# Kernel tuning notes

Measured on AMD Instinct MI355X. Metric: run time of the kernel, lower is better.

Reference implementation:

```python
import jax, jax.numpy as jnp
import numpy as np

B = 32          # claims
EVI = 5         # evidences per claim
L = 130         # max_len
H = 768         # bert_hidden_dim
K = 21          # n gaussian kernels
NL = 3          # num_labels
N = B * EVI


def _kernel_mus(n):
    mu = [1.0]
    bs = 2.0 / (n - 1)
    mu.append(1.0 - bs / 2.0)
    for i in range(1, n - 1):
        mu.append(mu[i] - bs)
    return mu


def _kernel_sigmas(n):
    return [0.001] + [0.1] * (n - 1)

MU = jnp.asarray(_kernel_mus(K), jnp.float32)      # [K]
SIGMA = jnp.asarray(_kernel_sigmas(K), jnp.float32)  # [K]


def _l2norm(x):
    # F.normalize(p=2, dim=-1, eps=1e-12)
    return x / jnp.maximum(jnp.linalg.norm(x, axis=-1, keepdims=True), 1e-12)


def _kernel_pool(sim, attn_d):
    # sim: [P, Q, D] cosine sims; attn_d: [P, D] doc mask -> [P, Q, K]
    pv = jnp.exp(-0.5 * ((sim[..., None] - MU) / SIGMA) ** 2) * attn_d[:, None, :, None]
    return pv.sum(axis=2)


def setup_inputs() -> dict:
    key = jax.random.key(0)
    ks = jax.random.split(key, 10)
    def p(k, shape, s=0.02):
        return jax.random.normal(k, shape, jnp.float32) * s
    return dict(
        hiddens=jax.random.normal(ks[0], (N, L, H), jnp.float32),
        pooled=jax.random.normal(ks[1], (N, H), jnp.float32),
        msk=jnp.ones((N, L), jnp.int32),
        seg=jax.random.randint(ks[2], (N, L), 0, 2, dtype=jnp.int32),
        W_att=p(ks[3], (1, K)), b_att=jnp.zeros((1,), jnp.float32),
        W_sel=p(ks[4], (1, K)), b_sel=jnp.zeros((1,), jnp.float32),
        Wg1=p(ks[5], (128, 2 * H)), bg1=jnp.zeros((128,), jnp.float32),
        Wg2=p(ks[6], (1, 128)), bg2=jnp.zeros((1,), jnp.float32),
        Wd=p(ks[7], (NL, 2 * H)), bd=jnp.zeros((NL,), jnp.float32),
    )


def reference(hiddens, pooled, msk, seg, W_att, b_att, W_sel, b_sel,
              Wg1, bg1, Wg2, bg2, Wd, bd):
    mask_text = msk.astype(jnp.float32).at[:, 0].set(0.0)       # [N,L] zero CLS
    segf = seg.astype(jnp.float32)
    mask_claim = (1.0 - segf) * mask_text
    mask_ev = segf * mask_text

    hn = _l2norm(hiddens)                                        # [N,L,H]

    # --- evidence selection: claim-vs-evidence kernel pooling within each row ---
    sim = jnp.einsum('nqh,ndh->nqd', hn, hn)                     # [N,L,L]
    ps = _kernel_pool(sim, mask_ev)                              # [N,L,K]
    lps = jnp.log(jnp.clip(ps, 1e-10, None)) * mask_claim[:, :, None]
    lps = lps.sum(axis=1) / (mask_claim.sum(axis=1, keepdims=True) + 1e-10)  # [N,K]
    sel = lps @ W_sel.T + b_sel                                  # [N,1]
    select_prob = jax.nn.softmax(sel.reshape(B, EVI, 1), axis=1)

    hb = hiddens.reshape(B, EVI, L, H)
    hnb = hn.reshape(B, EVI, L, H)
    mb = mask_text.reshape(B, EVI, L)
    pb = pooled.reshape(B, EVI, H)

    def proj_gat(x):
        return jnp.maximum(x @ Wg1.T + bg1, 0.0) @ Wg2.T + bg2

    # --- GAT-style aggregation; only the denoised branch feeds the output ---
    de_list = []
    for i in range(EVI):
        own_n = hnb[:, i]                                        # [B,L,H]
        own_m = jnp.repeat(mb[:, i], EVI, axis=0)                # [B*EVI,L]
        sim_i = jnp.einsum('beqh,bdh->beqd', hnb, own_n).reshape(B * EVI, L, L)
        ps_i = _kernel_pool(sim_i, own_m)                        # [B*EVI,L,K]
        score = (jnp.log(jnp.clip(ps_i, 1e-10, None)) @ W_att.T + b_att)[..., 0]
        score = jnp.where(mb.reshape(B * EVI, L) > 0, score, -10000.0)
        att = jax.nn.softmax(score, axis=1).reshape(B, EVI, L, 1)
        denoise = (att * hb).sum(axis=2)                         # [B,EVI,H]
        own_inp = jnp.broadcast_to(pb[:, i:i + 1], (B, EVI, H))
        w_de = jax.nn.softmax(proj_gat(jnp.concatenate([own_inp, denoise], -1)), axis=1)
        de_list.append((denoise * w_de).sum(axis=1))             # [B,H]

    de = jnp.stack(de_list, axis=1)                              # [B,EVI,H]
    feat = jnp.concatenate([pb, de], axis=-1) @ Wd.T + bd        # [B,EVI,NL]
    class_prob = jax.nn.softmax(feat, axis=2)
    prob = (select_prob * class_prob).sum(axis=1)                # [B,NL]
    return jnp.log(prob)
```

## Files before the change

### kernel.cpp

```cpp
#include <hip/hip_runtime.h>
#include <cstdint>
#include <cstddef>

#define BB 32
#define EV 5
#define LL 130
#define HH 768
#define KK 21
#define LP 160
#define SD 136
#define SR 130

typedef __attribute__((ext_vector_type(8))) __bf16 bf16x8;
typedef __attribute__((ext_vector_type(4))) float f32x4;

__device__ __forceinline__ unsigned short f2bf(float f) {
    unsigned int u = __float_as_uint(f);
    u += 0x7FFFu + ((u >> 16) & 1u);
    return (unsigned short)(u >> 16);
}
__device__ __forceinline__ float bf2f(unsigned int s) {
    return __uint_as_float(s << 16);
}
__device__ __forceinline__ void gld_lds16(const unsigned short* g, unsigned short* l) {
    __builtin_amdgcn_global_load_lds(
        (const __attribute__((address_space(1))) unsigned int*)g,
        (__attribute__((address_space(3))) unsigned int*)l, 16, 0, 0);
}

__global__ __launch_bounds__(256) void k_prologue(const float* __restrict__ hid,
        unsigned short* __restrict__ hnbf, const float* __restrict__ wg1,
        unsigned short* __restrict__ wg1b, const float* __restrict__ pooled,
        unsigned short* __restrict__ xg) {
    int bid = blockIdx.x, tid = threadIdx.x;
    if (bid < 5200) {
        int wave = tid >> 6, lane = tid & 63;
        int r = bid * 4 + wave;
        if (r >= 160 * LL) return;
        const float4* s4 = (const float4*)(hid + (size_t)r * HH);
        float4 v0 = s4[lane], v1 = s4[lane + 64], v2 = s4[lane + 128];
        float ss = v0.x*v0.x + v0.y*v0.y + v0.z*v0.z + v0.w*v0.w
                 + v1.x*v1.x + v1.y*v1.y + v1.z*v1.z + v1.w*v1.w
                 + v2.x*v2.x + v2.y*v2.y + v2.z*v2.z + v2.w*v2.w;
        #pragma unroll
        for (int m = 1; m < 64; m <<= 1) ss += __shfl_xor(ss, m, 64);
        float sc = 1.0f / fmaxf(sqrtf(ss), 1e-12f);
        ushort4 o0, o1, o2;
        o0.x = f2bf(v0.x*sc); o0.y = f2bf(v0.y*sc); o0.z = f2bf(v0.z*sc); o0.w = f2bf(v0.w*sc);
        o1.x = f2bf(v1.x*sc); o1.y = f2bf(v1.y*sc); o1.z = f2bf(v1.z*sc); o1.w = f2bf(v1.w*sc);
        o2.x = f2bf(v2.x*sc); o2.y = f2bf(v2.y*sc); o2.z = f2bf(v2.z*sc); o2.w = f2bf(v2.w*sc);
        ushort4* d4 = (ushort4*)(hnbf + (size_t)r * HH);
        d4[lane] = o0; d4[lane + 64] = o1; d4[lane + 128] = o2;
    } else if (bid < 5968) {
        int idx = (bid - 5200) * 256 + tid;
        wg1b[idx] = f2bf(wg1[idx]);
    } else {
        int row = bid - 5968;
        int bi = row / 5;
        const float* src = pooled + (size_t)bi * HH;
        unsigned short* dst = xg + (size_t)row * 1536;
        #pragma unroll
        for (int j = 0; j < 3; j++) { int h = tid + j * 256; dst[h] = f2bf(src[h]); }
    }
}

__global__ __launch_bounds__(256) void k_sim_gemm(const unsigned short* __restrict__ hnbf,
                                                  unsigned short* __restrict__ Sg) {
    int w = blockIdx.x;
    int xcd = w & 7, slot = w >> 3;
    int b = xcd * 4 + (slot / 25);
    int ei = slot % 25;
    int e = ei / 5, i = ei % 5;
    int pair = b * 25 + ei;
    const unsigned short* A = hnbf + (size_t)(b * 5 + e) * LL * HH;
    const unsigned short* B = hnbf + (size_t)(b * 5 + i) * LL * HH;
    __shared__ unsigned short As[160 * 64];
    __shared__ unsigned short Bs[160 * 64];
    int tid = threadIdx.x, lane = tid & 63, wave = tid >> 6;
    int quad = lane >> 4, l16 = lane & 15;
    int wm = (wave & 1) * 5, wn = (wave >> 1) * 5;
    f32x4 acc[5][5];
    #pragma unroll
    for (int mt = 0; mt < 5; mt++)
        #pragma unroll
        for (int nt = 0; nt < 5; nt++) acc[mt][nt] = (f32x4){0.f, 0.f, 0.f, 0.f};

    for (int k0 = 0; k0 < HH; k0 += 64) {
        #pragma unroll
        for (int it = 0; it < 5; it++) {
            int s = tid + it * 256;
            int r = s >> 3;
            int rs = (r < LL) ? r : 0;
            int sgl = (s & 7) ^ (r & 7);
            const unsigned short* ga = A + (size_t)rs * HH + k0 + sgl * 8;
            const unsigned short* gb = B + (size_t)rs * HH + k0 + sgl * 8;
            gld_lds16(ga, &As[s * 8]);
            gld_lds16(gb, &Bs[s * 8]);
        }
        __syncthreads();
        #pragma unroll
        for (int kb = 0; kb < 2; kb++) {
            bf16x8 af[5], bfr[5];
            #pragma unroll
            for (int t = 0; t < 5; t++) {
                int ra = (wm + t) * 16 + l16;
                int rb = (wn + t) * 16 + l16;
                af[t]  = *(const bf16x8*)&As[ra * 64 + (((kb << 2) + quad) ^ (ra & 7)) * 8];
                bfr[t] = *(const bf16x8*)&Bs[rb * 64 + (((kb << 2) + quad) ^ (rb & 7)) * 8];
            }
            #pragma unroll
            for (int mt = 0; mt < 5; mt++)
                #pragma unroll
                for (int nt = 0; nt < 5; nt++)
                    acc[mt][nt] = __builtin_amdgcn_mfma_f32_16x16x32_bf16(af[mt], bfr[nt], acc[mt][nt], 0, 0, 0);
        }
        __syncthreads();
    }
    size_t base = (size_t)pair * SR * SD;
    #pragma unroll
    for (int mt = 0; mt < 5; mt++)
        #pragma unroll
        for (int nt = 0; nt < 5; nt++) {
            int R0 = (wm + mt) * 16 + quad * 4;
            int C = (wn + nt) * 16 + l16;
            if (C < SD) {
                #pragma unroll
                for (int reg = 0; reg < 4; reg++) {
                    int R = R0 + reg;
                    if (R < SR) Sg[base + (size_t)R * SD + C] = f2bf(acc[mt][nt][reg]);
                }
            }
        }
}

template <bool DIAG>
__device__ __forceinline__ void pool_body(
    int pair, int row, int lane8, bool live, int ne, int c,
    const unsigned short* __restrict__ Sg,
    const float* __restrict__ batt,
    float* __restrict__ score, float* __restrict__ selp, float* __restrict__ denp,
    const float* wdA, const float* wdE, const float* wqC,
    const float* WaL, const float* WsL, const float* CkL,
    float* redsel, float* redden) {

    const float LOG2E = 1.4426950408889634f;
    const float CA = -50.0f * LOG2E;
    const float CB = 95.0f * LOG2E;
    const float CR = -10.0f * LOG2E;
    const float C0 = -500000.0f * LOG2E;
    int tid = threadIdx.x;

    float a0[KK], a2[KK];
    #pragma unroll
    for (int k = 0; k < KK; k++) { a0[k] = 0.0f; a2[k] = 0.0f; }

    auto proc = [&](float s, int d) {
        float w = wdA[d];
        float w2 = DIAG ? wdE[d] : 0.0f;
        float pe = exp2f(fmaf(CB, s, CA * s * s));
        float rr = exp2f(CR * s);
        float sm1 = s - 1.0f;
        float e0 = exp2f(C0 * (sm1 * sm1));
        a0[0] = fmaf(w, e0, a0[0]);
        if (DIAG) a2[0] = fmaf(w2, e0, a2[0]);
        float p = pe;
        #pragma unroll
        for (int k = 1; k < KK; k++) {
            a0[k] = fmaf(w, p, a0[k]);
            if (DIAG) a2[k] = fmaf(w2, p, a2[k]);
            p *= rr;
        }
    };

    if (live) {
        const unsigned short* Srow = Sg + (size_t)pair * SR * SD + (size_t)row * SD;
        #pragma unroll
        for (int j = 0; j < 2; j++) {
            uint4 v = *(const uint4*)(Srow + lane8 * 8 + j * 64);
            int d0 = lane8 * 8 + j * 64;
            proc(bf2f(v.x & 0xFFFFu), d0 + 0); proc(bf2f(v.x >> 16), d0 + 1);
            proc(bf2f(v.y & 0xFFFFu), d0 + 2); proc(bf2f(v.y >> 16), d0 + 3);
            proc(bf2f(v.z & 0xFFFFu), d0 + 4); proc(bf2f(v.z >> 16), d0 + 5);
            proc(bf2f(v.w & 0xFFFFu), d0 + 6); proc(bf2f(v.w >> 16), d0 + 7);
        }
        proc(bf2f((unsigned int)Srow[128 + lane8]), 128 + lane8);
    }
    #pragma unroll
    for (int k = 0; k < KK; k++) {
        a0[k] += __shfl_xor(a0[k], 1, 64);
        a0[k] += __shfl_xor(a0[k], 2, 64);
        a0[k] += __shfl_xor(a0[k], 4, 64);
        if (DIAG) {
            a2[k] += __shfl_xor(a2[k], 1, 64);
            a2[k] += __shfl_xor(a2[k], 2, 64);
            a2[k] += __shfl_xor(a2[k], 4, 64);
        }
    }
    float selv = 0.0f, denv = 0.0f;
    if (live && lane8 == 0) {
        float sc = batt[0];
        #pragma unroll
        for (int k = 0; k < KK; k++)
            sc += WaL[k] * __logf(fmaxf(CkL[k] * a0[k], 1e-10f));
        score[(size_t)pair * LP + row] = sc;
        if (DIAG) {
            float cq = 0.0f;
            #pragma unroll
            for (int k = 0; k < KK; k++)
                cq += WsL[k] * __logf(fmaxf(CkL[k] * a2[k], 1e-10f));
            selv = wqC[row] * cq;
            denv = wqC[row];
        }
    }
    if (DIAG) {
        #pragma unroll
        for (int m = 8; m < 64; m <<= 1) {
            selv += __shfl_xor(selv, m, 64);
            denv += __shfl_xor(denv, m, 64);
        }
        int wave = tid >> 6, lane = tid & 63;
        if (lane == 0) { redsel[wave] = selv; redden[wave] = denv; }
        __syncthreads();
        if (tid == 0) {
            selp[ne * 5 + c] = redsel[0] + redsel[1] + redsel[2] + redsel[3];
            denp[ne * 5 + c] = redden[0] + redden[1] + redden[2] + redden[3];
        }
    }
}

__global__ __launch_bounds__(256) void k_pool(const unsigned short* __restrict__ Sg,
        const int* __restrict__ msk, const int* __restrict__ seg,
        const float* __restrict__ Watt, const float* __restrict__ batt,
        const float* __restrict__ Wsel,
        float* __restrict__ score, float* __restrict__ selp, float* __restrict__ denp) {
    __shared__ float wdA[SD], wdE[SD], wqC[SD];
    __shared__ float WaL[KK], WsL[KK], CkL[KK];
    __shared__ float redsel[4], redden[4];
    int w = blockIdx.x;
    int xcd = w & 7, slot = w >> 3;
    int b = xcd * 4 + (slot / 125);
    int rem = slot % 125;
    int ei = rem / 5, c = rem % 5;
    int e = ei / 5, i = ei % 5;
    int pair = b * 25 + ei;
    int ne = b * 5 + e, ni = b * 5 + i;
    int tid = threadIdx.x;

    if (tid < SD) {
        int d = tid;
        wdA[d] = (d >= 1 && d < LL) ? (float)msk[ni * LL + d] : 0.0f;
        float mtE = (d >= 1 && d < LL) ? (float)msk[ne * LL + d] : 0.0f;
        float sgE = (d < LL) ? (float)seg[ne * LL + d] : 0.0f;
        wdE[d] = sgE * mtE;
        wqC[d] = (1.0f - sgE) * mtE;
    }
    if (tid < KK) {
        const float LOG2E = 1.4426950408889634f;
        WaL[tid] = Watt[tid];
        WsL[tid] = Wsel[tid];
        float mu = 0.95f - 0.1f * (tid - 1);
        CkL[tid] = (tid == 0) ? 1.0f : exp2f(-50.0f * LOG2E * mu * mu);
    }
    __syncthreads();

    int row = c * 26 + (tid >> 3);
    int lane8 = tid & 7;
    bool live = (tid < 208);

    if (e == i)
        pool_body<true>(pair, row, lane8, live, ne, c, Sg, batt, score, selp, denp,
                        wdA, wdE, wqC, WaL, WsL, CkL, redsel, redden);
    else
        pool_body<false>(pair, row, lane8, live, ne, c, Sg, batt, score, selp, denp,
                         wdA, wdE, wqC, WaL, WsL, CkL, redsel, redden);
}

__global__ __launch_bounds__(64) void k_att(const float* __restrict__ score,
        const int* __restrict__ msk, float* __restrict__ attg) {
    int bid = blockIdx.x;
    int be = bid / 5, ii = bid % 5;
    int b = be / 5, e = be % 5;
    const float* srow = score + ((size_t)(b * 5 + ii) * 5 + e) * LP;
    int lane = threadIdx.x;

    float v0, v1, v2 = -1e30f;
    {
        int q = lane;
        float mt = (q >= 1 && msk[be * LL + q] != 0) ? 1.0f : 0.0f;
        v0 = (mt > 0.0f) ? srow[q] : -1e4f;
    }
    {
        int q = lane + 64;
        float mt = (msk[be * LL + q] != 0) ? 1.0f : 0.0f;
        v1 = (mt > 0.0f) ? srow[q] : -1e4f;
    }
    if (lane < 2) {
        int q = lane + 128;
        float mt = (msk[be * LL + q] != 0) ? 1.0f : 0.0f;
        v2 = (mt > 0.0f) ? srow[q] : -1e4f;
    }
    float mx = fmaxf(v0, fmaxf(v1, v2));
    #pragma unroll
    for (int m = 1; m < 64; m <<= 1) mx = fmaxf(mx, __shfl_xor(mx, m, 64));
    float e0 = __expf(v0 - mx), e1 = __expf(v1 - mx);
    float e2 = (lane < 2) ? __expf(v2 - mx) : 0.0f;
    float Z = e0 + e1 + e2;
    #pragma unroll
    for (int m = 1; m < 64; m <<= 1) Z += __shfl_xor(Z, m, 64);
    float iz = 1.0f / Z;
    attg[(size_t)bid * LL + lane] = e0 * iz;
    attg[(size_t)bid * LL + lane + 64] = e1 * iz;
    if (lane < 2) attg[(size_t)bid * LL + lane + 128] = e2 * iz;
}

__global__ __launch_bounds__(256) void k_den(const float* __restrict__ attg,
        const float* __restrict__ hid, float* __restrict__ dn,
        unsigned short* __restrict__ xg) {
    int bid = blockIdx.x;
    int be = bid / 3, j = bid % 3;
    int b = be / 5, e = be % 5;
    int tid = threadIdx.x;
    int h = j * 256 + tid;
    __shared__ float attl[5 * LL];
    for (int s = tid; s < 5 * LL; s += 256)
        attl[s] = attg[(size_t)(be * 5) * LL + s];
    __syncthreads();

    float accA[5] = {0.f, 0.f, 0.f, 0.f, 0.f};
    float accB[5] = {0.f, 0.f, 0.f, 0.f, 0.f};
    const float* hb = hid + (size_t)be * LL * HH + h;
    int q = 0;
    #pragma unroll 2
    for (; q + 4 <= LL; q += 4) {
        float h0 = hb[(size_t)(q + 0) * HH];
        float h1 = hb[(size_t)(q + 1) * HH];
        float h2 = hb[(size_t)(q + 2) * HH];
        float h3 = hb[(size_t)(q + 3) * HH];
        #pragma unroll
        for (int i = 0; i < 5; i++) {
            accA[i] = fmaf(attl[i * LL + q], h0, accA[i]);
            accB[i] = fmaf(attl[i * LL + q + 1], h1, accB[i]);
            accA[i] = fmaf(attl[i * LL + q + 2], h2, accA[i]);
            accB[i] = fmaf(attl[i * LL + q + 3], h3, accB[i]);
        }
    }
    for (; q < LL; q++) {
        float hv = hb[(size_t)q * HH];
        #pragma unroll
        for (int i = 0; i < 5; i++) accA[i] = fmaf(attl[i * LL + q], hv, accA[i]);
    }
    #pragma unroll
    for (int i = 0; i < 5; i++) {
        float v = accA[i] + accB[i];
        dn[((size_t)be * 5 + i) * HH + h] = v;
        xg[((size_t)(b * 5 + i) * 5 + e) * 1536 + HH + h] = f2bf(v);
    }
}

__global__ __launch_bounds__(256) void k_gate_gemm(const unsigned short* __restrict__ xg,
        const unsigned short* __restrict__ wg1b, float* __restrict__ cg) {
    int bid = blockIdx.x;
    int rb = bid / 3, ks = bid % 3;
    int m0 = rb * 16;
    __shared__ unsigned short As[16 * 32];
    __shared__ unsigned short Bs[128 * 32];
    int tid = threadIdx.x, lane = tid & 63, wave = tid >> 6;
    int quad = lane >> 4, l16 = lane & 15;
    f32x4 acc[2];
    acc[0] = (f32x4){0.f, 0.f, 0.f, 0.f};
    acc[1] = (f32x4){0.f, 0.f, 0.f, 0.f};

    for (int t = 0; t < 16; t++) {
        int k0 = ks * 512 + t * 32;
        if (tid < 64) {
            int row = tid >> 2, sg = tid & 3;
            *(uint4*)&As[tid * 8] = *(const uint4*)(xg + (size_t)(m0 + row) * 1536 + k0 + sg * 8);
        }
        #pragma unroll
        for (int it = 0; it < 2; it++) {
            int s = tid + it * 256;
            int row = s >> 2, sg = s & 3;
            *(uint4*)&Bs[s * 8] = *(const uint4*)(wg1b + (size_t)row * 1536 + k0 + sg * 8);
        }
        __syncthreads();
        bf16x8 af = *(const bf16x8*)&As[l16 * 32 + quad * 8];
        #pragma unroll
        for (int nt = 0; nt < 2; nt++) {
            int ct = wave * 2 + nt;
            bf16x8 bfr = *(const bf16x8*)&Bs[(ct * 16 + l16) * 32 + quad * 8];
            acc[nt] = __builtin_amdgcn_mfma_f32_16x16x32_bf16(af, bfr, acc[nt], 0, 0, 0);
        }
        __syncthreads();
    }
    #pragma unroll
    for (int nt = 0; nt < 2; nt++) {
        int C = (wave * 2 + nt) * 16 + l16;
        #pragma unroll
        for (int reg = 0; reg < 4; reg++) {
            int R = m0 + quad * 4 + reg;
            atomicAdd(&cg[(size_t)R * 128 + C], acc[nt][reg]);
        }
    }
}

__global__ __launch_bounds__(256) void k_gate_epi(const float* __restrict__ cg,
        const float* __restrict__ bg1, const float* __restrict__ wg2,
        const float* __restrict__ bg2, const float* __restrict__ dn,
        const float* __restrict__ pooled, const float* __restrict__ wd,
        const float* __restrict__ bd, float* __restrict__ feat) {
    int bi = blockIdx.x;
    int b = bi / 5, ii = bi % 5;
    __shared__ float red4[4];
    __shared__ float gL[5];
    __shared__ float deL[HH];
    int tid = threadIdx.x, lane = tid & 63, wave = tid >> 6;

    for (int e = 0; e < 5; e++) {
        float v = 0.0f;
        if (tid < 128) {
            float ccv = cg[(size_t)(bi * 5 + e) * 128 + tid] + bg1[tid];
            v = wg2[tid] * fmaxf(ccv, 0.0f);
        }
        #pragma unroll
        for (int m = 1; m < 64; m <<= 1) v += __shfl_xor(v, m, 64);
        if (lane == 0) red4[wave] = v;
        __syncthreads();
        if (tid == 0) gL[e] = red4[0] + red4[1] + bg2[0];
        __syncthreads();
    }
    float mx = gL[0];
    #pragma unroll
    for (int e = 1; e < 5; e++) mx = fmaxf(mx, gL[e]);
    float wde[5]; float z = 0.0f;
    #pragma unroll
    for (int e = 0; e < 5; e++) { wde[e] = __expf(gL[e] - mx); z += wde[e]; }
    float iz = 1.0f / z;
    #pragma unroll
    for (int e = 0; e < 5; e++) wde[e] *= iz;

    #pragma unroll
    for (int j = 0; j < 3; j++) {
        int h = tid + j * 256;
        float v = 0.0f;
        #pragma unroll
        for (int e = 0; e < 5; e++)
            v += wde[e] * dn[((size_t)(b * 5 + e) * 5 + ii) * HH + h];
        deL[h] = v;
    }
    __syncthreads();

    float part[3] = {0.0f, 0.0f, 0.0f};
    #pragma unroll
    for (int mm = 0; mm < 6; mm++) {
        int h = tid + mm * 256;
        float x = (mm < 3) ? pooled[(size_t)bi * HH + h] : deL[h - HH];
        #pragma unroll
        for (int c = 0; c < 3; c++) part[c] = fmaf(x, wd[(size_t)c * 1536 + h], part[c]);
    }
    #pragma unroll
    for (int c = 0; c < 3; c++) {
        float v = part[c];
        #pragma unroll
        for (int m = 1; m < 64; m <<= 1) v += __shfl_xor(v, m, 64);
        if (lane == 0) red4[wave] = v;
        __syncthreads();
        if (tid == 0) feat[bi * 3 + c] = red4[0] + red4[1] + red4[2] + red4[3] + bd[c];
        __syncthreads();
    }
}

__global__ __launch_bounds__(64) void k_final(const float* __restrict__ selp,
        const float* __restrict__ denp, const float* __restrict__ bsel,
        const float* __restrict__ feat, float* __restrict__ out) {
    int b = threadIdx.x;
    if (b >= BB) return;
    float sv[5]; float m = -1e30f;
    #pragma unroll
    for (int i = 0; i < 5; i++) {
        float num = 0.0f, den = 0.0f;
        #pragma unroll
        for (int c = 0; c < 5; c++) {
            num += selp[(b * 5 + i) * 5 + c];
            den += denp[(b * 5 + i) * 5 + c];
        }
        sv[i] = bsel[0] + num / (den + 1e-10f);
        m = fmaxf(m, sv[i]);
    }
    float z = 0.0f;
    #pragma unroll
    for (int i = 0; i < 5; i++) { sv[i] = __expf(sv[i] - m); z += sv[i]; }
    #pragma unroll
    for (int i = 0; i < 5; i++) sv[i] /= z;
    float prob[3] = {0.0f, 0.0f, 0.0f};
    #pragma unroll
    for (int i = 0; i < 5; i++) {
        float f0 = feat[(b * 5 + i) * 3 + 0];
        float f1 = feat[(b * 5 + i) * 3 + 1];
        float f2 = feat[(b * 5 + i) * 3 + 2];
        float mm = fmaxf(f0, fmaxf(f1, f2));
        float e0 = __expf(f0 - mm), e1 = __expf(f1 - mm), e2 = __expf(f2 - mm);
        float zz = e0 + e1 + e2;
        prob[0] += sv[i] * e0 / zz;
        prob[1] += sv[i] * e1 / zz;
        prob[2] += sv[i] * e2 / zz;
    }
    #pragma unroll
    for (int c = 0; c < 3; c++) out[b * 3 + c] = __logf(prob[c]);
}

extern "C" void kernel_launch(void* const* d_in, const int* in_sizes, int n_in,
                              void* d_out, int out_size, void* d_ws, size_t ws_size,
                              hipStream_t stream) {
    const float* hiddens = (const float*)d_in[0];
    const float* pooled  = (const float*)d_in[1];
    const int*   msk     = (const int*)d_in[2];
    const int*   seg     = (const int*)d_in[3];
    const float* Watt    = (const float*)d_in[4];
    const float* batt    = (const float*)d_in[5];
    const float* Wsel    = (const float*)d_in[6];
    const float* bsel    = (const float*)d_in[7];
    const float* Wg1     = (const float*)d_in[8];
    const float* bg1     = (const float*)d_in[9];
    const float* Wg2     = (const float*)d_in[10];
    const float* bg2     = (const float*)d_in[11];
    const float* Wd      = (const float*)d_in[12];
    const float* bd      = (const float*)d_in[13];

    char* ws = (char*)d_ws;
    size_t off = 0;
    auto alloc = [&](size_t bytes) -> void* {
        void* p = ws + off;
        off += (bytes + 255) & ~(size_t)255;
        return p;
    };
    unsigned short* hnbf   = (unsigned short*)alloc((size_t)160 * LL * HH * 2);
    unsigned short* Sg     = (unsigned short*)alloc((size_t)800 * SR * SD * 2);
    float*          score  = (float*)alloc((size_t)800 * LP * 4);
    float*          selp   = (float*)alloc((size_t)160 * 5 * 4);
    float*          denp   = (float*)alloc((size_t)160 * 5 * 4);
    float*          attg   = (float*)alloc((size_t)800 * LL * 4);
    float*          dn     = (float*)alloc((size_t)160 * 5 * HH * 4);
    unsigned short* xg     = (unsigned short*)alloc((size_t)800 * 1536 * 2);
    unsigned short* wg1b   = (unsigned short*)alloc((size_t)128 * 1536 * 2);
    float*          cg     = (float*)alloc((size_t)800 * 128 * 4);
    float*          feat   = (float*)alloc((size_t)800 * 3 * 4);
    (void)ws_size; (void)in_sizes; (void)n_in; (void)out_size;

    hipMemsetAsync(cg, 0, (size_t)800 * 128 * 4, stream);
    k_prologue<<<dim3(6768), dim3(256), 0, stream>>>(hiddens, hnbf, Wg1, wg1b, pooled, xg);
    k_sim_gemm<<<dim3(800), dim3(256), 0, stream>>>(hnbf, Sg);
    k_pool<<<dim3(4000), dim3(256), 0, stream>>>(Sg, msk, seg, Watt, batt, Wsel, score, selp, denp);
    k_att<<<dim3(800), dim3(64), 0, stream>>>(score, msk, attg);
    k_den<<<dim3(480), dim3(256), 0, stream>>>(attg, hiddens, dn, xg);
    k_gate_gemm<<<dim3(150), dim3(256), 0, stream>>>(xg, wg1b, cg);
    k_gate_epi<<<dim3(160), dim3(256), 0, stream>>>(cg, bg1, Wg2, bg2, dn, pooled, Wd, bd, feat);
    k_final<<<dim3(1), dim3(64), 0, stream>>>(selp, denp, bsel, feat, (float*)d_out);
}
```

Before: 281.3 us.

## Load MFMA operands directly from global memory in sim GEMM, drop LDS staging

The similarity GEMM no longer stages A/B tiles through LDS with global_load_lds and barriers. Each lane now reads its bf16x8 fragments straight from global memory (relying on L1/L2 for reuse) inside a fully unrolled K loop, and the launch bounds ask for 3 blocks per CU. This removes the LDS traffic and __syncthreads, but each wave re-fetches operand rows from cache, adding global load pressure. It also risks register spills from the full unroll under the tighter occupancy target.

```diff
diff --git a/kernel.cpp b/kernel.cpp
--- a/kernel.cpp
+++ b/kernel.cpp
@@ -21,11 +21,6 @@
 }
 __device__ __forceinline__ float bf2f(unsigned int s) {
     return __uint_as_float(s << 16);
-}
-__device__ __forceinline__ void gld_lds16(const unsigned short* g, unsigned short* l) {
-    __builtin_amdgcn_global_load_lds(
-        (const __attribute__((address_space(1))) unsigned int*)g,
-        (__attribute__((address_space(3))) unsigned int*)l, 16, 0, 0);
 }
 
 __global__ __launch_bounds__(256) void k_prologue(const float* __restrict__ hid,
@@ -64,8 +59,8 @@
     }
 }
 
-__global__ __launch_bounds__(256) void k_sim_gemm(const unsigned short* __restrict__ hnbf,
-                                                  unsigned short* __restrict__ Sg) {
+__global__ __launch_bounds__(256, 3) void k_sim_gemm(const unsigned short* __restrict__ hnbf,
+                                                     unsigned short* __restrict__ Sg) {
     int w = blockIdx.x;
     int xcd = w & 7, slot = w >> 3;
     int b = xcd * 4 + (slot / 25);
@@ -74,48 +69,42 @@
     int pair = b * 25 + ei;
     const unsigned short* A = hnbf + (size_t)(b * 5 + e) * LL * HH;
     const unsigned short* B = hnbf + (size_t)(b * 5 + i) * LL * HH;
-    __shared__ unsigned short As[160 * 64];
-    __shared__ unsigned short Bs[160 * 64];
     int tid = threadIdx.x, lane = tid & 63, wave = tid >> 6;
     int quad = lane >> 4, l16 = lane & 15;
     int wm = (wave & 1) * 5, wn = (wave >> 1) * 5;
+
+    const unsigned short* aptr[5];
+    const unsigned short* bptr[5];
+    #pragma unroll
+    for (int t = 0; t < 5; t++) {
+        int ra = (wm + t) * 16 + l16; if (ra >= LL) ra = 0;
+        int rb = (wn + t) * 16 + l16; if (rb >= LL) rb = 0;
+        aptr[t] = A + (size_t)ra * HH + quad * 8;
+        bptr[t] = B + (size_t)rb * HH + quad * 8;
+    }
+
     f32x4 acc[5][5];
     #pragma unroll
     for (int mt = 0; mt < 5; mt++)
         #pragma unroll
         for (int nt = 0; nt < 5; nt++) acc[mt][nt] = (f32x4){0.f, 0.f, 0.f, 0.f};
 
-    for (int k0 = 0; k0 < HH; k0 += 64) {
-        #pragma unroll
-        for (int it = 0; it < 5; it++) {
-            int s = tid + it * 256;
-            int r = s >> 3;
-            int rs = (r < LL) ? r : 0;
-            int sgl = (s & 7) ^ (r & 7);
-            const unsigned short* ga = A + (size_t)rs * HH + k0 + sgl * 8;
-            const unsigned short* gb = B + (size_t)rs * HH + k0 + sgl * 8;
-            gld_lds16(ga, &As[s * 8]);
-            gld_lds16(gb, &Bs[s * 8]);
-        }
-        __syncthreads();
-        #pragma unroll
-        for (int kb = 0; kb < 2; kb++) {
-            bf16x8 af[5], bfr[5];
+    #pragma unroll
+    for (int ks = 0; ks < HH / 32; ks++) {
+        const int k0 = ks * 32;
+        bf16x8 af[5], bfr[5];
+        #pragma unroll
+        for (int t = 0; t < 5; t++) {
+            af[t]  = *(const bf16x8*)(aptr[t] + k0);
+            bfr[t] = *(const bf16x8*)(bptr[t] + k0);
+        }
+        #pragma unroll
+        for (int mt = 0; mt < 5; mt++)
             #pragma unroll
-            for (int t = 0; t < 5; t++) {
-                int ra = (wm + t) * 16 + l16;
-                int rb = (wn + t) * 16 + l16;
-                af[t]  = *(const bf16x8*)&As[ra * 64 + (((kb << 2) + quad) ^ (ra & 7)) * 8];
-                bfr[t] = *(const bf16x8*)&Bs[rb * 64 + (((kb << 2) + quad) ^ (rb & 7)) * 8];
-            }
-            #pragma unroll
-            for (int mt = 0; mt < 5; mt++)
-                #pragma unroll
-                for (int nt = 0; nt < 5; nt++)
-                    acc[mt][nt] = __builtin_amdgcn_mfma_f32_16x16x32_bf16(af[mt], bfr[nt], acc[mt][nt], 0, 0, 0);
-        }
-        __syncthreads();
-    }
+            for (int nt = 0; nt < 5; nt++)
+                acc[mt][nt] = __builtin_amdgcn_mfma_f32_16x16x32_bf16(af[mt], bfr[nt], acc[mt][nt], 0, 0, 0);
+    }
+
     size_t base = (size_t)pair * SR * SD;
     #pragma unroll
     for (int mt = 0; mt < 5; mt++)
```

Result: slower. 317.2 us (+12.8%).
